# Kernel tuning notes

Hardware: AMD Instinct MI355X
Metric: run time of the kernel (lower is better)

## Reference

```python
import jax, jax.numpy as jnp
import numpy as np

D_MODEL = 768
D_HEAD = 64
N_HEADS = D_MODEL // D_HEAD


def setup_inputs() -> dict:
    key = jax.random.key(0)
    k1, k2, k3 = jax.random.split(key, 3)
    n, h, w = 2, 48, 48
    x = jax.random.normal(k1, (n, h, w, D_MODEL), dtype=jnp.float32)
    # torch Linear weights: [out_features, in_features]
    w_qkv = jax.random.normal(k2, (3 * D_MODEL, D_MODEL), dtype=jnp.float32) * (D_MODEL ** -0.5)
    w_out = jax.random.normal(k3, (D_MODEL, D_MODEL), dtype=jnp.float32) * (D_MODEL ** -0.5)
    return {"x": x, "w_qkv": w_qkv, "w_out": w_out, "kernel_size": 7}


def _natten_mask(h: int, w: int, kernel_size: int) -> jnp.ndarray:
    # Faithful to _natten_mask_mod: q_x = idx // w, q_y = idx % w,
    # both axes compared against the same kernel_size.
    idx = jnp.arange(h * w)
    qx, qy = idx // w, idx % w
    horiz = jnp.abs(qx[:, None] - qx[None, :]) <= kernel_size
    vert = jnp.abs(qy[:, None] - qy[None, :]) <= kernel_size
    return horiz & vert  # [hw, hw] bool


def reference(x, w_qkv, w_out, kernel_size):
    n, h, w, d = x.shape
    hw = h * w
    qkv = jnp.einsum('nhwd,fd->nhwf', x, w_qkv)  # [n, h, w, 3*d]
    qkv = qkv.reshape(n, hw, 3, N_HEADS, D_HEAD)
    q = jnp.transpose(qkv[:, :, 0], (0, 2, 1, 3))  # [n, nh, hw, e]
    k = jnp.transpose(qkv[:, :, 1], (0, 2, 1, 3))
    v = jnp.transpose(qkv[:, :, 2], (0, 2, 1, 3))

    mask = _natten_mask(h, w, kernel_size)  # [hw, hw]
    scale = D_HEAD ** -0.5
    scores = jnp.einsum('bnqe,bnke->bnqk', q, k) * scale
    neg = jnp.asarray(jnp.finfo(scores.dtype).min, scores.dtype)
    scores = jnp.where(mask[None, None], scores, neg)
    attn = jax.nn.softmax(scores, axis=-1)
    o = jnp.einsum('bnqk,bnke->bnqe', attn, v)  # [n, nh, hw, e]
    o = jnp.transpose(o, (0, 2, 1, 3)).reshape(n, h, w, d)
    return jnp.einsum('nhwd,fd->nhwf', o, w_out)
```

## Files before the change

### kernel.cpp

```cpp
#include <hip/hip_runtime.h>

using f32x4 = __attribute__((ext_vector_type(4))) float;
using h8v   = __attribute__((ext_vector_type(8))) _Float16;
using h4v   = __attribute__((ext_vector_type(4))) _Float16;
using s8v   = __attribute__((ext_vector_type(8))) short;

#define MFMAH(a, b, c)   __builtin_amdgcn_mfma_f32_16x16x32_f16((a), (b), (c), 0, 0, 0)
#define MFMAH16(a, b, c) __builtin_amdgcn_mfma_f32_16x16x16f16((a), (b), (c), 0, 0, 0)

typedef __attribute__((address_space(3))) unsigned int lds_uint;
typedef const __attribute__((address_space(1))) unsigned int glb_uint;
__device__ inline void gload16(void* l, const void* g) {
    __builtin_amdgcn_global_load_lds((glb_uint*)g, (lds_uint*)l, 16, 0, 0);
}

__global__ __launch_bounds__(256) void conv_all(const float* __restrict__ x,
                                                const float* __restrict__ wq,
                                                const float* __restrict__ wo,
                                                _Float16* __restrict__ xh,
                                                _Float16* __restrict__ wqh,
                                                _Float16* __restrict__ woh) {
    const int i = blockIdx.x * blockDim.x + threadIdx.x;
    const float* src;
    _Float16* dst;
    int off;
    if (i < 442368)      { src = x;  dst = xh;  off = i; }
    else if (i < 663552) { src = wq; dst = wqh; off = i - 442368; }
    else                 { src = wo; dst = woh; off = i - 663552; }
    const float4 a = *(const float4*)(src + (size_t)off * 8);
    const float4 b = *(const float4*)(src + (size_t)off * 8 + 4);
    h8v h;
    h[0] = (_Float16)a.x; h[1] = (_Float16)a.y; h[2] = (_Float16)a.z; h[3] = (_Float16)a.w;
    h[4] = (_Float16)b.x; h[5] = (_Float16)b.y; h[6] = (_Float16)b.z; h[7] = (_Float16)b.w;
    *(h8v*)(dst + (size_t)off * 8) = h;
}

__global__ __launch_bounds__(256) void gemm_qkv_f16(const _Float16* __restrict__ A,
                                                    const _Float16* __restrict__ B,
                                                    _Float16* __restrict__ C) {
    constexpr int LD = 768, LDC = 2304;
    __shared__ __align__(16) _Float16 sA[128][32], sB[128][32];
    const int b = blockIdx.x;
    const int sb = (b & 7) * 81 + (b >> 3);
    const int bx = sb % 18, by = sb / 18;
    const int m0 = by * 128, n0 = bx * 128;
    const int tid = threadIdx.x, lane = tid & 63, wv = tid >> 6;
    const int wm = (wv >> 1) * 64, wn = (wv & 1) * 64;
    const int fr = lane & 15, fkb = (lane >> 4) * 8;

    const int srow = tid >> 2, scol = (tid & 3) * 8;
    const _Float16* gA = A + (size_t)(m0 + srow) * LD + scol;
    const _Float16* gB = B + (size_t)(n0 + srow) * LD + scol;

    f32x4 acc[4][4];
#pragma unroll
    for (int m = 0; m < 4; ++m)
#pragma unroll
        for (int n2 = 0; n2 < 4; ++n2) acc[m][n2] = (f32x4){0.f, 0.f, 0.f, 0.f};

    for (int kt = 0; kt < 24; ++kt) {
        const int k0 = kt * 32;
        gload16(&sA[srow][scol],      gA + k0);
        gload16(&sA[64 + srow][scol], gA + 64 * LD + k0);
        gload16(&sB[srow][scol],      gB + k0);
        gload16(&sB[64 + srow][scol], gB + 64 * LD + k0);
        __syncthreads();

        h8v fa[4], fb[4];
#pragma unroll
        for (int m = 0; m < 4; ++m) fa[m] = *(const h8v*)&sA[wm + m * 16 + fr][fkb];
#pragma unroll
        for (int n2 = 0; n2 < 4; ++n2) fb[n2] = *(const h8v*)&sB[wn + n2 * 16 + fr][fkb];
#pragma unroll
        for (int m = 0; m < 4; ++m)
#pragma unroll
            for (int n2 = 0; n2 < 4; ++n2) acc[m][n2] = MFMAH(fa[m], fb[n2], acc[m][n2]);
        __syncthreads();
    }

    const int rg = (lane >> 4) * 4;
#pragma unroll
    for (int m = 0; m < 4; ++m)
#pragma unroll
        for (int n2 = 0; n2 < 4; ++n2)
#pragma unroll
            for (int r = 0; r < 4; ++r)
                C[(size_t)(m0 + wm + m * 16 + rg + r) * LDC + (n0 + wn + n2 * 16 + fr)] =
                    (_Float16)acc[m][n2][r];
}

__global__ __launch_bounds__(256) void vtrans(const unsigned short* __restrict__ qkv,
                                              unsigned short* __restrict__ vt) {
    __shared__ unsigned short t[64][72];
    const int tt = blockIdx.x, head = blockIdx.y, n = blockIdx.z;
    const int tid = threadIdx.x;
#pragma unroll
    for (int i = 0; i < 2; ++i) {
        const int el = i * 2048 + tid * 8;
        const int tr = el >> 6, c = el & 63;
        s8v v = *(const s8v*)(qkv + (size_t)(n * 2304 + tt * 64 + tr) * 2304 + 1536 + head * 64 + c);
        *(s8v*)&t[tr][c] = v;
    }
    __syncthreads();
#pragma unroll
    for (int i = 0; i < 2; ++i) {
        const int el = i * 2048 + tid * 8;
        const int er = el >> 6, tk = el & 63;
        s8v w;
#pragma unroll
        for (int j = 0; j < 8; ++j) w[j] = (short)t[tk + j][er];
        *(s8v*)(vt + (size_t)((n * 12 + head) * 64 + er) * 2304 + tt * 64 + tk) = w;
    }
}

__global__ __launch_bounds__(192) void attn_flash(const _Float16* __restrict__ qkv,
                                                  const _Float16* __restrict__ vt,
                                                  _Float16* __restrict__ o,
                                                  const int* __restrict__ ksp) {
    __shared__ __align__(16) char sbuf[2][14336];
    const int tid = threadIdx.x;
    const int lane = tid & 63, wv = tid >> 6;
    const int fr = lane & 15, fg = lane >> 4;

    const int b = blockIdx.x;
    const int xcd = b & 7, g = b >> 3;
    const int qx = xcd * 6 + g / 24;
    const int hn = g % 24;
    const int head = hn >> 1, n = hn & 1;
    const int KS = *ksp;

    const int krow0 = tid >> 3, kc = tid & 7;
    const int vrow0 = tid / 6,  vc = tid % 6;
    const int ksw = (krow0 & 7) << 4;
    const int vsw = (vrow0 & 7) << 4;

    const int qy = wv * 16 + fr;
    const _Float16* qrow = qkv + (size_t)(n * 2304 + qx * 48 + qy) * 2304 + head * 64;
    h8v qa0 = *(const h8v*)(qrow + fg * 8);
    h8v qa1 = *(const h8v*)(qrow + 32 + fg * 8);
    qa0 = qa0 * (_Float16)0.125f;
    qa1 = qa1 * (_Float16)0.125f;

    int nt0 = (wv * 16 - KS) >> 4;      if (nt0 < 0) nt0 = 0;
    int nt1 = (wv * 16 + 15 + KS) >> 4; if (nt1 > 2) nt1 = 2;

    f32x4 Oacc[4];
#pragma unroll
    for (int e = 0; e < 4; ++e) Oacc[e] = (f32x4){0.f, 0.f, 0.f, 0.f};
    float mrow = -1e30f, rs_acc = 0.f;

    const int lo = (qx - KS) > 0 ? (qx - KS) : 0;
    const int hi = (qx + KS) < 47 ? (qx + KS) : 47;

    const _Float16* kgbase = qkv + (size_t)(n * 2304) * 2304 + 768 + head * 64;
    const _Float16* vgbase = vt + (size_t)((n * 12 + head) * 64) * 2304;

    {
        const _Float16* kg = kgbase + (size_t)(lo * 48) * 2304;
        const _Float16* vg = vgbase + lo * 48;
        const s8v a0 = *(const s8v*)(kg + (size_t)krow0 * 2304 + kc * 8);
        const s8v a1 = *(const s8v*)(kg + (size_t)(krow0 + 24) * 2304 + kc * 8);
        const s8v b0 = *(const s8v*)(vg + (size_t)vrow0 * 2304 + vc * 8);
        const s8v b1 = *(const s8v*)(vg + (size_t)(vrow0 + 32) * 2304 + vc * 8);
        *(s8v*)(sbuf[0] + krow0 * 128 + ((kc * 16) ^ ksw)) = a0;
        *(s8v*)(sbuf[0] + (krow0 + 24) * 128 + ((kc * 16) ^ ksw)) = a1;
        *(s8v*)(sbuf[0] + 6144 + vrow0 * 128 + ((vc * 16) ^ vsw)) = b0;
        *(s8v*)(sbuf[0] + 6144 + (vrow0 + 32) * 128 + ((vc * 16) ^ vsw)) = b1;
    }

    int p = 0;
    for (int kx = lo; kx <= hi; ++kx) {
        __syncthreads();
        const bool pre = (kx < hi);
        s8v tk0, tk1, tv0, tv1;
        if (pre) {
            const _Float16* kg = kgbase + (size_t)((kx + 1) * 48) * 2304;
            const _Float16* vg = vgbase + (kx + 1) * 48;
            tk0 = *(const s8v*)(kg + (size_t)krow0 * 2304 + kc * 8);
            tk1 = *(const s8v*)(kg + (size_t)(krow0 + 24) * 2304 + kc * 8);
            tv0 = *(const s8v*)(vg + (size_t)vrow0 * 2304 + vc * 8);
            tv1 = *(const s8v*)(vg + (size_t)(vrow0 + 32) * 2304 + vc * 8);
        }

        const char* K = sbuf[p];
        const char* V = sbuf[p] + 6144;

        f32x4 s[3];
#pragma unroll
        for (int nt = 0; nt < 3; ++nt)
            if (nt >= nt0 && nt <= nt1) {
                const int rr = nt * 16 + fr;
                const int sw = (rr & 7) << 4;
                const h8v kb0 = *(const h8v*)(K + rr * 128 + ((fg * 16) ^ sw));
                const h8v kb1 = *(const h8v*)(K + rr * 128 + ((64 + fg * 16) ^ sw));
                f32x4 z = (f32x4){0.f, 0.f, 0.f, 0.f};
                z = MFMAH(kb0, qa0, z);
                z = MFMAH(kb1, qa1, z);
                s[nt] = z;
            }

        float vmax = -1e30f;
#pragma unroll
        for (int nt = 0; nt < 3; ++nt)
            if (nt >= nt0 && nt <= nt1)
#pragma unroll
                for (int r = 0; r < 4; ++r) {
                    const int ky = nt * 16 + fg * 4 + r;
                    float v = s[nt][r];
                    const int dy = ky - qy;
                    if (dy < -KS || dy > KS) v = -1e30f;
                    s[nt][r] = v;
                    vmax = fmaxf(vmax, v);
                }

        if (!__all(vmax <= mrow + 8.f)) {
            float vm = fmaxf(vmax, __shfl_xor(vmax, 16));
            vm = fmaxf(vm, __shfl_xor(vm, 32));
            const float mn = fmaxf(mrow, vm);
            const float sf = __expf(mrow - mn);
            mrow = mn;
            rs_acc *= sf;
#pragma unroll
            for (int et = 0; et < 4; ++et)
#pragma unroll
                for (int r = 0; r < 4; ++r) Oacc[et][r] *= sf;
        }

#pragma unroll
        for (int nt = 0; nt < 3; ++nt)
            if (nt >= nt0 && nt <= nt1) {
                h4v pa;
#pragma unroll
                for (int r = 0; r < 4; ++r) {
                    const float pv = __expf(s[nt][r] - mrow);
                    rs_acc += pv;
                    pa[r] = (_Float16)pv;
                }
                const int slot = nt * 2 + (fg >> 1), off8 = (fg & 1) * 8;
#pragma unroll
                for (int et = 0; et < 4; ++et) {
                    const int rv = et * 16 + fr;
                    const h4v vb = *(const h4v*)(V + rv * 128 +
                                                 (((slot ^ (rv & 7)) << 4) + off8));
                    Oacc[et] = MFMAH16(vb, pa, Oacc[et]);
                }
            }

        if (pre) {
            char* d = sbuf[p ^ 1];
            *(s8v*)(d + krow0 * 128 + ((kc * 16) ^ ksw)) = tk0;
            *(s8v*)(d + (krow0 + 24) * 128 + ((kc * 16) ^ ksw)) = tk1;
            *(s8v*)(d + 6144 + vrow0 * 128 + ((vc * 16) ^ vsw)) = tv0;
            *(s8v*)(d + 6144 + (vrow0 + 32) * 128 + ((vc * 16) ^ vsw)) = tv1;
        }
        p ^= 1;
    }

    rs_acc += __shfl_xor(rs_acc, 16);
    rs_acc += __shfl_xor(rs_acc, 32);
    const float linv = 1.f / rs_acc;
    _Float16* ob = o + (size_t)(n * 2304 + qx * 48 + wv * 16 + fr) * 768 + head * 64;
#pragma unroll
    for (int et = 0; et < 4; ++et) {
        h4v ov;
#pragma unroll
        for (int r = 0; r < 4; ++r) ov[r] = (_Float16)(Oacc[et][r] * linv);
        *(h4v*)(ob + et * 16 + fg * 4) = ov;
    }
}

__global__ __launch_bounds__(256) void gemm_out_f16(const _Float16* __restrict__ A,
                                                    const _Float16* __restrict__ B,
                                                    float* __restrict__ C) {
    constexpr int LD = 768, LDC = 768;
    __shared__ __align__(16) _Float16 sA[128][32], sB[128][32];
    const int b = blockIdx.x;
    const int sb = (b & 7) * 27 + (b >> 3);
    const int bx = sb % 6, by = sb / 6;
    const int m0 = by * 128, n0 = bx * 128;
    const int tid = threadIdx.x, lane = tid & 63, wv = tid >> 6;
    const int wm = (wv >> 1) * 64, wn = (wv & 1) * 64;
    const int fr = lane & 15, fkb = (lane >> 4) * 8;

    const int srow = tid >> 2, scol = (tid & 3) * 8;
    const _Float16* gA = A + (size_t)(m0 + srow) * LD + scol;
    const _Float16* gB = B + (size_t)(n0 + srow) * LD + scol;

    f32x4 acc[4][4];
#pragma unroll
    for (int m = 0; m < 4; ++m)
#pragma unroll
        for (int n2 = 0; n2 < 4; ++n2) acc[m][n2] = (f32x4){0.f, 0.f, 0.f, 0.f};

    for (int kt = 0; kt < 24; ++kt) {
        const int k0 = kt * 32;
        gload16(&sA[srow][scol],      gA + k0);
        gload16(&sA[64 + srow][scol], gA + 64 * LD + k0);
        gload16(&sB[srow][scol],      gB + k0);
        gload16(&sB[64 + srow][scol], gB + 64 * LD + k0);
        __syncthreads();

        h8v fa[4], fb[4];
#pragma unroll
        for (int m = 0; m < 4; ++m) fa[m] = *(const h8v*)&sA[wm + m * 16 + fr][fkb];
#pragma unroll
        for (int n2 = 0; n2 < 4; ++n2) fb[n2] = *(const h8v*)&sB[wn + n2 * 16 + fr][fkb];
#pragma unroll
        for (int m = 0; m < 4; ++m)
#pragma unroll
            for (int n2 = 0; n2 < 4; ++n2) acc[m][n2] = MFMAH(fa[m], fb[n2], acc[m][n2]);
        __syncthreads();
    }

    const int rg = (lane >> 4) * 4;
#pragma unroll
    for (int m = 0; m < 4; ++m)
#pragma unroll
        for (int n2 = 0; n2 < 4; ++n2)
#pragma unroll
            for (int r = 0; r < 4; ++r)
                C[(size_t)(m0 + wm + m * 16 + rg + r) * LDC + (n0 + wn + n2 * 16 + fr)] =
                    acc[m][n2][r];
}

extern "C" void kernel_launch(void* const* d_in, const int* in_sizes, int n_in,
                              void* d_out, int out_size, void* d_ws, size_t ws_size,
                              hipStream_t stream) {
    const float* x     = (const float*)d_in[0];
    const float* w_qkv = (const float*)d_in[1];
    const float* w_out = (const float*)d_in[2];
    const int*   ksp   = (const int*)d_in[3];
    float* out = (float*)d_out;

    char* ws = (char*)d_ws;
    _Float16* qkv = (_Float16*)(ws);
    _Float16* vt  = (_Float16*)(ws + 21237760);
    _Float16* o   = (_Float16*)(ws + 28315648);
    _Float16* xh  = (_Float16*)(ws + 35393536);
    _Float16* wqh = (_Float16*)(ws + 42471424);
    _Float16* woh = (_Float16*)(ws + 46010368);

    conv_all<<<dim3(2880), 256, 0, stream>>>(x, w_qkv, w_out, xh, wqh, woh);
    gemm_qkv_f16<<<dim3(648), 256, 0, stream>>>(xh, wqh, qkv);
    vtrans<<<dim3(36, 12, 2), 256, 0, stream>>>((const unsigned short*)qkv,
                                                (unsigned short*)vt);
    attn_flash<<<dim3(1152), 192, 0, stream>>>(qkv, vt, o, ksp);
    gemm_out_f16<<<dim3(216), 256, 0, stream>>>(o, woh, out);
}
```

Before: 90.53 us.

## Double GEMM K-tile, use exp2 softmax, and hoist V fragment loads in attention

Both fp16 GEMMs now stage a 64-wide K slice per iteration instead of 32. That halves the number of barrier pairs and loop trips, at the cost of twice the LDS. The attention kernel folds log2(e) into the query scale and calls the raw v_exp_f32 instruction instead of __expf, with the rescale threshold raised to match the base-2 domain. V fragments are now loaded from LDS before the softmax so the reads can overlap the exponent math, which raises register pressure. The 128-byte row stride in the new LDS tiles may cause bank conflicts on fragment reads.

```diff
diff --git a/kernel.cpp b/kernel.cpp
--- a/kernel.cpp
+++ b/kernel.cpp
@@ -12,6 +12,12 @@
 typedef const __attribute__((address_space(1))) unsigned int glb_uint;
 __device__ inline void gload16(void* l, const void* g) {
     __builtin_amdgcn_global_load_lds((glb_uint*)g, (lds_uint*)l, 16, 0, 0);
+}
+
+__device__ inline float exp2_fast(float x) {
+    float r;
+    asm("v_exp_f32 %0, %1" : "=v"(r) : "v"(x));
+    return r;
 }
 
 __global__ __launch_bounds__(256) void conv_all(const float* __restrict__ x,
@@ -39,7 +45,7 @@
                                                     const _Float16* __restrict__ B,
                                                     _Float16* __restrict__ C) {
     constexpr int LD = 768, LDC = 2304;
-    __shared__ __align__(16) _Float16 sA[128][32], sB[128][32];
+    __shared__ __align__(16) _Float16 sA[128][64], sB[128][64];
     const int b = blockIdx.x;
     const int sb = (b & 7) * 81 + (b >> 3);
     const int bx = sb % 18, by = sb / 18;
@@ -48,7 +54,7 @@
     const int wm = (wv >> 1) * 64, wn = (wv & 1) * 64;
     const int fr = lane & 15, fkb = (lane >> 4) * 8;
 
-    const int srow = tid >> 2, scol = (tid & 3) * 8;
+    const int srow = tid >> 3, scol = (tid & 7) * 8;
     const _Float16* gA = A + (size_t)(m0 + srow) * LD + scol;
     const _Float16* gB = B + (size_t)(n0 + srow) * LD + scol;
 
@@ -58,23 +64,27 @@
 #pragma unroll
         for (int n2 = 0; n2 < 4; ++n2) acc[m][n2] = (f32x4){0.f, 0.f, 0.f, 0.f};
 
-    for (int kt = 0; kt < 24; ++kt) {
-        const int k0 = kt * 32;
-        gload16(&sA[srow][scol],      gA + k0);
-        gload16(&sA[64 + srow][scol], gA + 64 * LD + k0);
-        gload16(&sB[srow][scol],      gB + k0);
-        gload16(&sB[64 + srow][scol], gB + 64 * LD + k0);
-        __syncthreads();
-
-        h8v fa[4], fb[4];
-#pragma unroll
-        for (int m = 0; m < 4; ++m) fa[m] = *(const h8v*)&sA[wm + m * 16 + fr][fkb];
-#pragma unroll
-        for (int n2 = 0; n2 < 4; ++n2) fb[n2] = *(const h8v*)&sB[wn + n2 * 16 + fr][fkb];
-#pragma unroll
-        for (int m = 0; m < 4; ++m)
-#pragma unroll
-            for (int n2 = 0; n2 < 4; ++n2) acc[m][n2] = MFMAH(fa[m], fb[n2], acc[m][n2]);
+    for (int kt = 0; kt < 12; ++kt) {
+        const int k0 = kt * 64;
+#pragma unroll
+        for (int q = 0; q < 4; ++q) {
+            gload16(&sA[q * 32 + srow][scol], gA + (size_t)(q * 32) * LD + k0);
+            gload16(&sB[q * 32 + srow][scol], gB + (size_t)(q * 32) * LD + k0);
+        }
+        __syncthreads();
+
+#pragma unroll
+        for (int kk = 0; kk < 2; ++kk) {
+            h8v fa[4], fb[4];
+#pragma unroll
+            for (int m = 0; m < 4; ++m) fa[m] = *(const h8v*)&sA[wm + m * 16 + fr][kk * 32 + fkb];
+#pragma unroll
+            for (int n2 = 0; n2 < 4; ++n2) fb[n2] = *(const h8v*)&sB[wn + n2 * 16 + fr][kk * 32 + fkb];
+#pragma unroll
+            for (int m = 0; m < 4; ++m)
+#pragma unroll
+                for (int n2 = 0; n2 < 4; ++n2) acc[m][n2] = MFMAH(fa[m], fb[n2], acc[m][n2]);
+        }
         __syncthreads();
     }
 
@@ -138,8 +148,8 @@
     const _Float16* qrow = qkv + (size_t)(n * 2304 + qx * 48 + qy) * 2304 + head * 64;
     h8v qa0 = *(const h8v*)(qrow + fg * 8);
     h8v qa1 = *(const h8v*)(qrow + 32 + fg * 8);
-    qa0 = qa0 * (_Float16)0.125f;
-    qa1 = qa1 * (_Float16)0.125f;
+    qa0 = qa0 * (_Float16)0.1803368801f;
+    qa1 = qa1 * (_Float16)0.1803368801f;
 
     int nt0 = (wv * 16 - KS) >> 4;      if (nt0 < 0) nt0 = 0;
     int nt1 = (wv * 16 + 15 + KS) >> 4; if (nt1 > 2) nt1 = 2;
@@ -199,6 +209,19 @@
                 s[nt] = z;
             }
 
+        h4v vbf[3][4];
+#pragma unroll
+        for (int nt = 0; nt < 3; ++nt)
+            if (nt >= nt0 && nt <= nt1) {
+                const int slot = nt * 2 + (fg >> 1), off8 = (fg & 1) * 8;
+#pragma unroll
+                for (int et = 0; et < 4; ++et) {
+                    const int rv = et * 16 + fr;
+                    vbf[nt][et] = *(const h4v*)(V + rv * 128 +
+                                                (((slot ^ (rv & 7)) << 4) + off8));
+                }
+            }
+
         float vmax = -1e30f;
 #pragma unroll
         for (int nt = 0; nt < 3; ++nt)
@@ -213,11 +236,11 @@
                     vmax = fmaxf(vmax, v);
                 }
 
-        if (!__all(vmax <= mrow + 8.f)) {
+        if (!__all(vmax <= mrow + 11.5f)) {
             float vm = fmaxf(vmax, __shfl_xor(vmax, 16));
             vm = fmaxf(vm, __shfl_xor(vm, 32));
             const float mn = fmaxf(mrow, vm);
-            const float sf = __expf(mrow - mn);
+            const float sf = exp2_fast(mrow - mn);
             mrow = mn;
             rs_acc *= sf;
 #pragma unroll
@@ -232,18 +255,13 @@
                 h4v pa;
 #pragma unroll
                 for (int r = 0; r < 4; ++r) {
-                    const float pv = __expf(s[nt][r] - mrow);
+                    const float pv = exp2_fast(s[nt][r] - mrow);
                     rs_acc += pv;
                     pa[r] = (_Float16)pv;
                 }
-                const int slot = nt * 2 + (fg >> 1), off8 = (fg & 1) * 8;
-#pragma unroll
-                for (int et = 0; et < 4; ++et) {
-                    const int rv = et * 16 + fr;
-                    const h4v vb = *(const h4v*)(V + rv * 128 +
-                                                 (((slot ^ (rv & 7)) << 4) + off8));
-                    Oacc[et] = MFMAH16(vb, pa, Oacc[et]);
-                }
+#pragma unroll
+                for (int et = 0; et < 4; ++et)
+                    Oacc[et] = MFMAH16(vbf[nt][et], pa, Oacc[et]);
             }
 
         if (pre) {
@@ -273,7 +291,7 @@
                                                     const _Float16* __restrict__ B,
                                                     float* __restrict__ C) {
     constexpr int LD = 768, LDC = 768;
-    __shared__ __align__(16) _Float16 sA[128][32], sB[128][32];
+    __shared__ __align__(16) _Float16 sA[128][64], sB[128][64];
     const int b = blockIdx.x;
     const int sb = (b & 7) * 27 + (b >> 3);
     const int bx = sb % 6, by = sb / 6;
@@ -282,7 +300,7 @@
     const int wm = (wv >> 1) * 64, wn = (wv & 1) * 64;
     const int fr = lane & 15, fkb = (lane >> 4) * 8;
 
-    const int srow = tid >> 2, scol = (tid & 3) * 8;
+    const int srow = tid >> 3, scol = (tid & 7) * 8;
     const _Float16* gA = A + (size_t)(m0 + srow) * LD + scol;
     const _Float16* gB = B + (size_t)(n0 + srow) * LD + scol;
 
@@ -292,23 +310,27 @@
 #pragma unroll
         for (int n2 = 0; n2 < 4; ++n2) acc[m][n2] = (f32x4){0.f, 0.f, 0.f, 0.f};
 
-    for (int kt = 0; kt < 24; ++kt) {
-        const int k0 = kt * 32;
-        gload16(&sA[srow][scol],      gA + k0);
-        gload16(&sA[64 + srow][scol], gA + 64 * LD + k0);
-        gload16(&sB[srow][scol],      gB + k0);
-        gload16(&sB[64 + srow][scol], gB + 64 * LD + k0);
-        __syncthreads();
-
-        h8v fa[4], fb[4];
-#pragma unroll
-        for (int m = 0; m < 4; ++m) fa[m] = *(const h8v*)&sA[wm + m * 16 + fr][fkb];
-#pragma unroll
-        for (int n2 = 0; n2 < 4; ++n2) fb[n2] = *(const h8v*)&sB[wn + n2 * 16 + fr][fkb];
-#pragma unroll
-        for (int m = 0; m < 4; ++m)
-#pragma unroll
-            for (int n2 = 0; n2 < 4; ++n2) acc[m][n2] = MFMAH(fa[m], fb[n2], acc[m][n2]);
+    for (int kt = 0; kt < 12; ++kt) {
+        const int k0 = kt * 64;
+#pragma unroll
+        for (int q = 0; q < 4; ++q) {
+            gload16(&sA[q * 32 + srow][scol], gA + (size_t)(q * 32) * LD + k0);
+            gload16(&sB[q * 32 + srow][scol], gB + (size_t)(q * 32) * LD + k0);
+        }
+        __syncthreads();
+
+#pragma unroll
+        for (int kk = 0; kk < 2; ++kk) {
+            h8v fa[4], fb[4];
+#pragma unroll
+            for (int m = 0; m < 4; ++m) fa[m] = *(const h8v*)&sA[wm + m * 16 + fr][kk * 32 + fkb];
+#pragma unroll
+            for (int n2 = 0; n2 < 4; ++n2) fb[n2] = *(const h8v*)&sB[wn + n2 * 16 + fr][kk * 32 + fkb];
+#pragma unroll
+            for (int m = 0; m < 4; ++m)
+#pragma unroll
+                for (int n2 = 0; n2 < 4; ++n2) acc[m][n2] = MFMAH(fa[m], fb[n2], acc[m][n2]);
+        }
         __syncthreads();
     }
 
```

Result: slower. 101.1 us (+11.7%).
